# Optimization experiments

Hardware: AMD Instinct MI355X
Metric: run time of the kernel (lower is better)

## Reference

```python
import jax, jax.numpy as jnp
import numpy as np

N_NODES = 20000
N_EDGES = 320000
N_GRAPHS = 512
N_FEAT = 29
DIMS = [N_FEAT, 1024, 512, 256, 512, 1024]
EPS = 1e-5


def setup_inputs() -> dict:
    key = jax.random.key(0)
    ks = jax.random.split(key, 32)
    inp = {}
    inp["x"] = jax.random.normal(ks[0], (N_NODES, N_FEAT), dtype=jnp.float32)
    inp["edge_index"] = jax.random.randint(ks[1], (2, N_EDGES), 0, N_NODES, dtype=jnp.int64)
    inp["batch"] = jnp.sort(jax.random.randint(ks[2], (N_NODES,), 0, N_GRAPHS, dtype=jnp.int64))
    # 5 GCNConv layers: weight [in, out] + bias, plus BN gamma/beta
    for i in range(5):
        din, dout = DIMS[i], DIMS[i + 1]
        inp[f"W{i+1}"] = jax.random.normal(ks[3 + i], (din, dout), dtype=jnp.float32) * (1.0 / np.sqrt(din))
        inp[f"b{i+1}"] = jnp.zeros((dout,), dtype=jnp.float32)
        inp[f"g{i+1}"] = jnp.ones((dout,), dtype=jnp.float32)
        inp[f"be{i+1}"] = jnp.zeros((dout,), dtype=jnp.float32)
    # attention gate Linear(1024, 1)
    inp["Wg"] = jax.random.normal(ks[10], (1024, 1), dtype=jnp.float32) * 0.03
    inp["bg"] = jnp.zeros((1,), dtype=jnp.float32)
    # MLP head
    inp["Wf2"] = jax.random.normal(ks[11], (1024, 128), dtype=jnp.float32) * 0.03
    inp["bf2"] = jnp.zeros((128,), dtype=jnp.float32)
    inp["Wf3"] = jax.random.normal(ks[12], (128, 16), dtype=jnp.float32) * 0.25
    inp["bf3"] = jnp.zeros((16,), dtype=jnp.float32)
    inp["Wf4"] = jax.random.normal(ks[13], (16, 1), dtype=jnp.float32) * 0.25
    inp["bf4"] = jnp.zeros((1,), dtype=jnp.float32)
    return inp


def _gcn_conv(x, row, col, W, b):
    # PyG GCNConv: linear transform, then D^{-1/2}(A+I)D^{-1/2} aggregation, then bias.
    n = x.shape[0]
    xw = x @ W  # [N, dout]
    deg = jax.ops.segment_sum(jnp.ones_like(col, dtype=xw.dtype), col, num_segments=n)
    dinv = jnp.where(deg > 0, jax.lax.rsqrt(deg), 0.0)
    norm = dinv[row] * dinv[col]  # [E+N]
    out = jax.ops.segment_sum(xw[row] * norm[:, None], col, num_segments=n)
    return out + b


def _bn_train(x, gamma, beta):
    m = jnp.mean(x, axis=0)
    v = jnp.var(x, axis=0)  # biased, matches torch training normalization
    return gamma * (x - m) * jax.lax.rsqrt(v + EPS) + beta


def _global_attention(x, batch, Wg, bg, n_graphs):
    gate = (x @ Wg + bg)[:, 0]  # [N]
    gmax = jax.ops.segment_max(gate, batch, num_segments=n_graphs)
    e = jnp.exp(gate - gmax[batch])
    s = jax.ops.segment_sum(e, batch, num_segments=n_graphs)
    alpha = e / s[batch]
    return jax.ops.segment_sum(alpha[:, None] * x, batch, num_segments=n_graphs)


def reference(x, edge_index, batch,
              W1, b1, g1, be1, W2, b2, g2, be2, W3, b3, g3, be3,
              W4, b4, g4, be4, W5, b5, g5, be5,
              Wg, bg, Wf2, bf2, Wf3, bf3, Wf4, bf4):
    n = x.shape[0]
    sl = jnp.arange(n, dtype=edge_index.dtype)
    row = jnp.concatenate([edge_index[0], sl])  # with self-loops
    col = jnp.concatenate([edge_index[1], sl])
    h = x
    params = [(W1, b1, g1, be1), (W2, b2, g2, be2), (W3, b3, g3, be3),
              (W4, b4, g4, be4), (W5, b5, g5, be5)]
    for (W, b, g, be) in params:
        h = jax.nn.relu(_gcn_conv(h, row, col, W, b))
        h = _bn_train(h, g, be)
    p = _global_attention(h, batch, Wg, bg, N_GRAPHS)  # [G, 1024]
    p = jax.nn.relu(p @ Wf2 + bf2)
    p = jax.nn.relu(p @ Wf3 + bf3)
    return p @ Wf4 + bf4  # [G, 1]
```

## Files before the change

kernel.cpp:

```cpp
#include <hip/hip_runtime.h>

#define EPS_BN 1e-5f

constexpr int NN   = 20000;
constexpr int NE   = 320000;
constexpr int NTOT = NE + NN;
constexpr int NG   = 512;
constexpr int MPAD = 20480;
constexpr int NBLK = 79;

typedef _Float16 half8  __attribute__((ext_vector_type(8)));
typedef _Float16 half2v __attribute__((ext_vector_type(2)));
typedef float floatx4   __attribute__((ext_vector_type(4)));

__global__ void k_deg(const int* __restrict__ col, int* __restrict__ deg,
                      const int* __restrict__ batch, int* __restrict__ gcnt) {
  int e = blockIdx.x * blockDim.x + threadIdx.x;
  if (e >= NTOT) return;
  int c = (e < NE) ? col[e] : (e - NE);
  atomicAdd(&deg[c], 1);
  if (e < NN) atomicAdd(&gcnt[batch[e]], 1);
}

__global__ __launch_bounds__(256) void k_pre1(const int* __restrict__ deg,
                                              float* __restrict__ dinvv,
                                              int* __restrict__ psum) {
  __shared__ int ws[4];
  int t = threadIdx.x, lane = t & 63, wv = t >> 6;
  int idx = blockIdx.x * 256 + t;
  int d = (idx < NN) ? deg[idx] : 0;
  if (idx < NN) dinvv[idx] = rsqrtf((float)d);
  int s = d;
  for (int o = 1; o < 64; o <<= 1) { int u = __shfl_up(s, o, 64); if (lane >= o) s += u; }
  if (lane == 63) ws[wv] = s;
  __syncthreads();
  if (t == 0) psum[blockIdx.x] = ws[0] + ws[1] + ws[2] + ws[3];
}

__global__ __launch_bounds__(256) void k_pre2(const int* __restrict__ psum,
                                              int* __restrict__ pbase,
                                              const int* __restrict__ gcnt,
                                              int* __restrict__ goff) {
  __shared__ int ws[8];
  int t = threadIdx.x, lane = t & 63, wv = t >> 6;
  int v = (t < NBLK) ? psum[t] : 0;
  int inc = v;
  for (int o = 1; o < 64; o <<= 1) { int u = __shfl_up(inc, o, 64); if (lane >= o) inc += u; }
  if (lane == 63) ws[wv] = inc;
  __syncthreads();
  int base = 0;
  for (int w = 0; w < wv; ++w) base += ws[w];
  int excl = base + inc - v;
  if (t < NBLK) pbase[t] = excl;
  if (t == NBLK - 1) pbase[NBLK] = excl + v;
  __syncthreads();
  int a0 = gcnt[2 * t], a1 = gcnt[2 * t + 1];
  int p = a0 + a1;
  int incp = p;
  for (int o = 1; o < 64; o <<= 1) { int u = __shfl_up(incp, o, 64); if (lane >= o) incp += u; }
  if (lane == 63) ws[4 + wv] = incp;
  __syncthreads();
  int gb = 0;
  for (int w = 0; w < wv; ++w) gb += ws[4 + w];
  int exclp = gb + incp - p;
  goff[2 * t]     = exclp;
  goff[2 * t + 1] = exclp + a0;
  if (t == 255) goff[NG] = exclp + p;
}

__global__ __launch_bounds__(256) void k_pre3(const int* __restrict__ deg,
                                              const int* __restrict__ pbase,
                                              int* __restrict__ indptr,
                                              int* __restrict__ cursor) {
  __shared__ int ws[4];
  int t = threadIdx.x, lane = t & 63, wv = t >> 6;
  int idx = blockIdx.x * 256 + t;
  int d = (idx < NN) ? deg[idx] : 0;
  int inc = d;
  for (int o = 1; o < 64; o <<= 1) { int u = __shfl_up(inc, o, 64); if (lane >= o) inc += u; }
  if (lane == 63) ws[wv] = inc;
  __syncthreads();
  int base = pbase[blockIdx.x];
  for (int w = 0; w < wv; ++w) base += ws[w];
  int excl = base + inc - d;
  if (idx < NN) { indptr[idx] = excl; cursor[idx] = excl; }
  if (idx == NN - 1) indptr[NN] = excl + d;
}

__global__ void k_fill(const int* __restrict__ row, const int* __restrict__ col,
                       const float* __restrict__ dinv, int* __restrict__ cursor,
                       int2* __restrict__ csw, float* __restrict__ rsum) {
  int e = blockIdx.x * blockDim.x + threadIdx.x;
  if (e >= NTOT) return;
  int r, c;
  if (e < NE) { r = row[e]; c = col[e]; } else { r = c = e - NE; }
  float wv = dinv[r] * dinv[c];
  int pos = atomicAdd(&cursor[c], 1);
  int2 m; m.x = r; m.y = __builtin_bit_cast(int, wv);
  csw[pos] = m;
  atomicAdd(&rsum[c], wv);
}

__device__ __forceinline__ size_t fragoff(int n, int k, int kb) {
  return ((size_t)(n >> 4) * kb + (k >> 5)) * 512 + ((k >> 3) & 3) * 128 + (n & 15) * 8;
}

__global__ void k_wconv3(const float* __restrict__ W0, const float* __restrict__ W3,
                         const float* __restrict__ W4,
                         _Float16* __restrict__ T0, _Float16* __restrict__ T3,
                         _Float16* __restrict__ T4) {
  int c = blockIdx.x * blockDim.x + threadIdx.x;
  _Float16 ov[8];
  if (c < 4096) {
    int n = c >> 2, k = (c & 3) * 8;
    #pragma unroll
    for (int i = 0; i < 8; ++i)
      ov[i] = (_Float16)((k + i < 29) ? W0[(size_t)(k + i) * 1024 + n] : 0.f);
    *(uint4*)&T0[fragoff(n, k, 1)] = *(const uint4*)ov;
  } else if (c < 4096 + 16384) {
    int c2 = c - 4096;
    int n = c2 >> 5, k = (c2 & 31) * 8;
    #pragma unroll
    for (int i = 0; i < 8; ++i)
      ov[i] = (_Float16)W3[(size_t)(k + i) * 512 + n];
    *(uint4*)&T3[fragoff(n, k, 8)] = *(const uint4*)ov;
  } else if (c < 4096 + 16384 + 65536) {
    int c3 = c - 20480;
    int n = c3 >> 6, k = (c3 & 63) * 8;
    #pragma unroll
    for (int i = 0; i < 8; ++i)
      ov[i] = (_Float16)W4[(size_t)(k + i) * 1024 + n];
    *(uint4*)&T4[fragoff(n, k, 16)] = *(const uint4*)ov;
  }
}

__global__ __launch_bounds__(256) void k_wfold(const float* __restrict__ W, int K, int N,
                                               const float* __restrict__ sums,
                                               const float* __restrict__ gamma,
                                               const float* __restrict__ beta,
                                               _Float16* __restrict__ T,
                                               float* __restrict__ c) {
  __shared__ float red[256];
  int n = blockIdx.x, tid = threadIdx.x;
  int kb = K >> 5;
  const float inv_n = 1.f / NN;
  float csum = 0.f;
  for (int kc = tid; kc < (K >> 3); kc += 256) {
    int k = kc * 8;
    _Float16 ov[8];
    #pragma unroll
    for (int i = 0; i < 8; ++i) {
      int ki = k + i;
      float mean = sums[ki] * inv_n;
      float var  = sums[K + ki] * inv_n - mean * mean;
      float sc   = gamma[ki] * rsqrtf(var + EPS_BN);
      float sh   = beta[ki] - mean * sc;
      float wv   = W[(size_t)ki * N + n];
      ov[i] = (_Float16)(sc * wv);
      csum += sh * wv;
    }
    *(uint4*)&T[fragoff(n, k, kb)] = *(const uint4*)ov;
  }
  red[tid] = csum;
  __syncthreads();
  for (int o = 128; o > 0; o >>= 1) {
    if (tid < o) red[tid] += red[tid + o];
    __syncthreads();
  }
  if (tid == 0) c[n] = red[0];
}

#define AGG_CH 128
__global__ __launch_bounds__(128) void k_agg29(
    const float* __restrict__ X,
    const int* __restrict__ indptr, const int2* __restrict__ csw,
    _Float16* __restrict__ Y) {
  __shared__ int   s_src[AGG_CH];
  __shared__ float s_w[AGG_CH];
  __shared__ float red[128];
  int node = blockIdx.x;
  int tid  = threadIdx.x;
  int sub  = tid / 29;
  int feat = tid - sub * 29;
  bool act = tid < 116;
  int beg = indptr[node], end = indptr[node + 1];
  float acc = 0.f;
  for (int e0 = beg; e0 < end; e0 += AGG_CH) {
    int c = min(AGG_CH, end - e0);
    if (tid < c) {
      int2 m = csw[e0 + tid];
      s_src[tid] = m.x;
      s_w[tid]   = __builtin_bit_cast(float, m.y);
    }
    __syncthreads();
    if (act) {
      for (int j = 0; j < c; j += 4) {
        int jj = j + sub;
        if (jj < c) acc += s_w[jj] * X[(size_t)s_src[jj] * 29 + feat];
      }
    }
    __syncthreads();
  }
  red[tid] = acc;
  __syncthreads();
  if (tid < 32) {
    float v = 0.f;
    if (tid < 29) v = red[tid] + red[29 + tid] + red[58 + tid] + red[87 + tid];
    size_t fb = (size_t)(node >> 4) * 512 + (size_t)(tid >> 3) * 128 + (node & 15) * 8 + (tid & 7);
    Y[fb] = (_Float16)v;
  }
}

template<int MODE>
__global__ __launch_bounds__(256) void k_aggv(
    const _Float16* __restrict__ X,
    _Float16* __restrict__ Yf, _Float16* __restrict__ Yrow,
    const int* __restrict__ indptr, const int2* __restrict__ csw,
    const float* __restrict__ rowsum,
    const float* __restrict__ p0, const float* __restrict__ p1,
    const float* __restrict__ p2)
{
  constexpr int F = 512;
  int wave = threadIdx.x >> 6;
  int lane = threadIdx.x & 63;
  int node = blockIdx.x * 4 + wave;
  int beg = indptr[node], end = indptr[node + 1];
  float acc[8];
  #pragma unroll
  for (int i = 0; i < 8; ++i) acc[i] = 0.f;
  const unsigned* Xl = (const unsigned*)X + lane * 4;

  auto body = [&](int e) {
    int2 m = csw[e];
    float we = __builtin_bit_cast(float, m.y);
    uint4 d = *(const uint4*)(Xl + (size_t)m.x * (F / 2));
    unsigned uu[4] = {d.x, d.y, d.z, d.w};
    #pragma unroll
    for (int i = 0; i < 4; ++i) {
      half2v h = __builtin_bit_cast(half2v, uu[i]);
      acc[2 * i]     = fmaf(we, (float)h[0], acc[2 * i]);
      acc[2 * i + 1] = fmaf(we, (float)h[1], acc[2 * i + 1]);
    }
  };
  int e = beg;
  for (; e + 8 <= end; e += 8) {
    body(e); body(e + 1); body(e + 2); body(e + 3);
    body(e + 4); body(e + 5); body(e + 6); body(e + 7);
  }
  for (; e < end; ++e) body(e);

  float s_n = rowsum[node];
  _Float16 outv[8];
  #pragma unroll
  for (int i = 0; i < 8; ++i) {
    int f = lane * 8 + i;
    float v;
    if constexpr (MODE == 0) {
      v = fmaxf(acc[i] + s_n * p0[f] + p1[f], 0.f);
    } else {
      const float inv_n = 1.f / NN;
      float mean = p0[f] * inv_n;
      float var  = p0[F + f] * inv_n - mean * mean;
      float sc   = p1[f] * rsqrtf(var + EPS_BN);
      float sh   = p2[f] - mean * sc;
      v = sc * acc[i] + s_n * sh;
    }
    outv[i] = (_Float16)v;
  }
  if (Yf) {
    size_t fb = (size_t)(node >> 4) * (16 * 512) + lane * 128 + (node & 15) * 8;
    *(uint4*)(Yf + fb) = *(const uint4*)outv;
  }
  if (Yrow) {
    *(uint4*)(Yrow + (size_t)node * F + lane * 8) = *(const uint4*)outv;
  }
}

template<int MODE>
__global__ __launch_bounds__(256) void k_aggp(
    const _Float16* __restrict__ X,
    _Float16* __restrict__ Yf, _Float16* __restrict__ Yrow,
    const int* __restrict__ indptr, const int2* __restrict__ csw,
    const float* __restrict__ rowsum,
    const float* __restrict__ p0, const float* __restrict__ p1,
    const float* __restrict__ p2)
{
  constexpr int F = 256;
  int wave = threadIdx.x >> 6;
  int lane = threadIdx.x & 63;
  int half = lane >> 5;
  int l32  = lane & 31;
  int node = blockIdx.x * 8 + wave * 2 + half;
  int beg = indptr[node], end = indptr[node + 1];
  int len = end - beg;
  int len0 = __shfl(len, 0, 64);
  int len1 = __shfl(len, 32, 64);
  int maxlen = max(len0, len1);

  float acc[8];
  #pragma unroll
  for (int i = 0; i < 8; ++i) acc[i] = 0.f;
  const unsigned* Xl = (const unsigned*)X + l32 * 4;

  auto body = [&](int t) {
    int e = beg + min(t, len - 1);
    int2 m = csw[e];
    float we = (t < len) ? __builtin_bit_cast(float, m.y) : 0.f;
    uint4 d = *(const uint4*)(Xl + (size_t)m.x * (F / 2));
    unsigned uu[4] = {d.x, d.y, d.z, d.w};
    #pragma unroll
    for (int i = 0; i < 4; ++i) {
      half2v h = __builtin_bit_cast(half2v, uu[i]);
      acc[2 * i]     = fmaf(we, (float)h[0], acc[2 * i]);
      acc[2 * i + 1] = fmaf(we, (float)h[1], acc[2 * i + 1]);
    }
  };
  int t = 0;
  for (; t + 4 <= maxlen; t += 4) { body(t); body(t + 1); body(t + 2); body(t + 3); }
  for (; t < maxlen; ++t) body(t);

  float s_n = rowsum[node];
  _Float16 outv[8];
  #pragma unroll
  for (int i = 0; i < 8; ++i) {
    int f = l32 * 8 + i;
    float v;
    if constexpr (MODE == 0) {
      v = fmaxf(acc[i] + s_n * p0[f] + p1[f], 0.f);
    } else {
      const float inv_n = 1.f / NN;
      float mean = p0[f] * inv_n;
      float var  = p0[F + f] * inv_n - mean * mean;
      float sc   = p1[f] * rsqrtf(var + EPS_BN);
      float sh   = p2[f] - mean * sc;
      v = sc * acc[i] + s_n * sh;
    }
    outv[i] = (_Float16)v;
  }
  if (Yf) {
    size_t fb = (size_t)(node >> 4) * (8 * 512) + l32 * 128 + (node & 15) * 8;
    *(uint4*)(Yf + fb) = *(const uint4*)outv;
  }
  if (Yrow) {
    *(uint4*)(Yrow + (size_t)node * F + l32 * 8) = *(const uint4*)outv;
  }
}

template<int K, int FRAGOUT>
__global__ __launch_bounds__(256) void k_gemmf(
    const _Float16* __restrict__ Af, const _Float16* __restrict__ Bf,
    const float* __restrict__ bias,
    _Float16* __restrict__ Ch,
    _Float16* __restrict__ Cf,
    float* __restrict__ stats,
    int N, int do_relu, int nbx)
{
  __shared__ __align__(16) _Float16 cs[128 * 136];
  __shared__ float sred[256];

  const int tid  = threadIdx.x;
  const int wave = tid >> 6;
  const int lane = tid & 63;

  int lin = blockIdx.x;
  int xcd = lin & 7, seq = lin >> 3;
  int bx = seq % nbx, grp = seq / nbx;
  int by = xcd + 8 * grp;
  const int row0 = by * 128;
  const int col0 = bx * 128;

  const int q  = lane >> 4;
  const int mm = lane & 15;
  const int wm = wave >> 1;
  const int wn = wave & 1;

  sred[tid] = 0.f;

  constexpr int KB = K / 32;
  const _Float16* pa[4];
  const _Float16* pb[4];
  #pragma unroll
  for (int i = 0; i < 4; ++i)
    pa[i] = Af + (size_t)((row0 >> 4) + wm * 4 + i) * (KB * 512) + lane * 8;
  #pragma unroll
  for (int j = 0; j < 4; ++j)
    pb[j] = Bf + (size_t)((col0 >> 4) + wn * 4 + j) * (KB * 512) + lane * 8;

  floatx4 acc[4][4];
  #pragma unroll
  for (int i = 0; i < 4; ++i)
    #pragma unroll
    for (int j = 0; j < 4; ++j) acc[i][j] = floatx4{0.f, 0.f, 0.f, 0.f};

  half8 av[4], bv[4];
  #pragma unroll
  for (int i = 0; i < 4; ++i) { av[i] = *(const half8*)pa[i]; pa[i] += 512; }
  #pragma unroll
  for (int j = 0; j < 4; ++j) { bv[j] = *(const half8*)pb[j]; pb[j] += 512; }

  #pragma unroll 2
  for (int s = 0; s < KB; ++s) {
    half8 nav[4], nbv[4];
    if (s + 1 < KB) {
      #pragma unroll
      for (int i = 0; i < 4; ++i) { nav[i] = *(const half8*)pa[i]; pa[i] += 512; }
      #pragma unroll
      for (int j = 0; j < 4; ++j) { nbv[j] = *(const half8*)pb[j]; pb[j] += 512; }
    }
    #pragma unroll
    for (int j = 0; j < 4; ++j)
      #pragma unroll
      for (int i = 0; i < 4; ++i)
        acc[i][j] = __builtin_amdgcn_mfma_f32_16x16x32_f16(av[i], bv[j], acc[i][j], 0, 0, 0);
    if (s + 1 < KB) {
      #pragma unroll
      for (int i = 0; i < 4; ++i) av[i] = nav[i];
      #pragma unroll
      for (int j = 0; j < 4; ++j) bv[j] = nbv[j];
    }
  }

  __syncthreads();

  float sloc[4]  = {0.f, 0.f, 0.f, 0.f};
  float s2loc[4] = {0.f, 0.f, 0.f, 0.f};
  #pragma unroll
  for (int j = 0; j < 4; ++j) {
    int cl = wn * 64 + j * 16 + mm;
    float bvv = bias ? bias[col0 + cl] : 0.f;
    #pragma unroll
    for (int i = 0; i < 4; ++i) {
      #pragma unroll
      for (int r = 0; r < 4; ++r) {
        int rl = wm * 64 + i * 16 + q * 4 + r;
        float v = acc[i][j][r] + bvv;
        if (do_relu) v = fmaxf(v, 0.f);
        cs[rl * 136 + cl] = (_Float16)v;
        if (row0 + rl < NN) { sloc[j] += v; s2loc[j] += v * v; }
      }
    }
  }

  if (stats) {
    #pragma unroll
    for (int j = 0; j < 4; ++j) {
      float a = sloc[j], b2 = s2loc[j];
      a  += __shfl_xor(a, 16, 64);  a  += __shfl_xor(a, 32, 64);
      b2 += __shfl_xor(b2, 16, 64); b2 += __shfl_xor(b2, 32, 64);
      if (q == 0) {
        int cl = wn * 64 + j * 16 + mm;
        atomicAdd(&sred[cl], a);
        atomicAdd(&sred[128 + cl], b2);
      }
    }
  }
  __syncthreads();

  if (FRAGOUT) {
    int mlo = tid & 15, sub = (tid >> 4) & 3, kcr = (tid >> 6) & 3;
    int kbN = N >> 5;
    #pragma unroll
    for (int pass = 0; pass < 8; ++pass) {
      int m = pass * 16 + mlo;
      int kl = kcr * 32 + sub * 8;
      uint4 d = *(const uint4*)&cs[m * 136 + kl];
      size_t fa = ((size_t)((row0 >> 4) + pass) * kbN + (col0 >> 5) + kcr) * 512
                + sub * 128 + mlo * 8;
      *(uint4*)&Cf[fa] = d;
    }
  } else {
    #pragma unroll
    for (int pass = 0; pass < 8; ++pass) {
      int cidx = tid + pass * 256;
      int r = cidx >> 4, kc = cidx & 15;
      int rr = row0 + r;
      if (rr < NN) {
        uint4 d = *(const uint4*)&cs[r * 136 + kc * 8];
        *(uint4*)&Ch[(size_t)rr * N + col0 + kc * 8] = d;
      }
    }
  }

  if (stats && tid < 128) {
    atomicAdd(&stats[col0 + tid], sred[tid]);
    atomicAdd(&stats[N + col0 + tid], sred[128 + tid]);
  }
}

template<int F>
__global__ __launch_bounds__(256) void k_statsf(const _Float16* __restrict__ Xf,
                                                float* __restrict__ sums) {
  constexpr int KB = F / 32;
  constexpr int NT = NN / 16;
  int wid  = (blockIdx.x * 256 + threadIdx.x) >> 6;
  int lane = threadIdx.x & 63;
  int nw   = (gridDim.x * 256) >> 6;
  int kidx = wid % KB;
  int ng0  = wid / KB;
  int step = nw / KB;
  int sub = lane >> 4, n16 = lane & 15;

  float s[8], s2[8];
  #pragma unroll
  for (int i = 0; i < 8; ++i) { s[i] = 0.f; s2[i] = 0.f; }

  for (int ng = ng0; ng < NT; ng += step) {
    const _Float16* p = Xf + ((size_t)ng * KB + kidx) * 512 + lane * 8;
    uint4 d = *(const uint4*)p;
    unsigned uu[4] = {d.x, d.y, d.z, d.w};
    #pragma unroll
    for (int i = 0; i < 4; ++i) {
      half2v h = __builtin_bit_cast(half2v, uu[i]);
      float v0 = (float)h[0], v1 = (float)h[1];
      s[2 * i]      += v0;  s2[2 * i]     += v0 * v0;
      s[2 * i + 1]  += v1;  s2[2 * i + 1] += v1 * v1;
    }
  }
  #pragma unroll
  for (int o = 1; o < 16; o <<= 1) {
    #pragma unroll
    for (int i = 0; i < 8; ++i) {
      s[i]  += __shfl_xor(s[i],  o, 64);
      s2[i] += __shfl_xor(s2[i], o, 64);
    }
  }
  if (n16 == 0) {
    int f = kidx * 32 + sub * 8;
    #pragma unroll
    for (int i = 0; i < 8; ++i) {
      atomicAdd(&sums[f + i], s[i]);
      atomicAdd(&sums[F + f + i], s2[i]);
    }
  }
}

__global__ __launch_bounds__(256) void k_stats16(const _Float16* __restrict__ X, int F,
                                                 float* __restrict__ sums) {
  int tid = threadIdx.x;
  int npf = F >> 8;
  float s[2] = {0.f, 0.f}, s2[2] = {0.f, 0.f};
  for (int r = blockIdx.x; r < NN; r += gridDim.x) {
    #pragma unroll
    for (int i = 0; i < 2; ++i) {
      if (i < npf) {
        float v = (float)X[(size_t)r * F + tid + i * 256];
        s[i] += v; s2[i] += v * v;
      }
    }
  }
  #pragma unroll
  for (int i = 0; i < 2; ++i) {
    if (i < npf) {
      atomicAdd(&sums[tid + i * 256], s[i]);
      atomicAdd(&sums[F + tid + i * 256], s2[i]);
    }
  }
}

__global__ __launch_bounds__(256) void k_gfold(const float* __restrict__ sums,
                                               const float* __restrict__ g5,
                                               const float* __restrict__ be5,
                                               const float* __restrict__ Wg,
                                               const float* __restrict__ bg,
                                               float* __restrict__ wgf,
                                               float* __restrict__ cg) {
  __shared__ float red[256];
  int tid = threadIdx.x;
  const float inv_n = 1.f / NN;
  float t = 0.f;
  #pragma unroll
  for (int i = 0; i < 4; ++i) {
    int f = i * 256 + tid;
    float mean = sums[f] * inv_n;
    float var  = sums[1024 + f] * inv_n - mean * mean;
    float sc   = g5[f] * rsqrtf(var + EPS_BN);
    float sh   = be5[f] - mean * sc;
    float wv   = Wg[f];
    wgf[f] = sc * wv;
    t += sh * wv;
  }
  red[tid] = t;
  __syncthreads();
  for (int o = 128; o > 0; o >>= 1) {
    if (tid < o) red[tid] += red[tid + o];
    __syncthreads();
  }
  if (tid == 0) cg[0] = red[0] + bg[0];
}

__global__ __launch_bounds__(256) void k_gate3(const _Float16* __restrict__ X,
                                               const float* __restrict__ wgf,
                                               const float* __restrict__ cg,
                                               float* __restrict__ gate) {
  int wave = threadIdx.x >> 6, lane = threadIdx.x & 63;
  int node = blockIdx.x * 4 + wave;
  const _Float16* xp = X + (size_t)node * 1024 + lane * 16;
  uint4 d0 = *(const uint4*)xp;
  uint4 d1 = *(const uint4*)(xp + 8);
  const float4* wp = (const float4*)(wgf + lane * 16);
  float4 w0 = wp[0], w1 = wp[1], w2 = wp[2], w3 = wp[3];
  float wv[16] = {w0.x, w0.y, w0.z, w0.w, w1.x, w1.y, w1.z, w1.w,
                  w2.x, w2.y, w2.z, w2.w, w3.x, w3.y, w3.z, w3.w};
  unsigned uu[8] = {d0.x, d0.y, d0.z, d0.w, d1.x, d1.y, d1.z, d1.w};
  float s = 0.f;
  #pragma unroll
  for (int i = 0; i < 8; ++i) {
    half2v h = __builtin_bit_cast(half2v, uu[i]);
    s = fmaf((float)h[0], wv[2 * i],     s);
    s = fmaf((float)h[1], wv[2 * i + 1], s);
  }
  #pragma unroll
  for (int o = 1; o < 64; o <<= 1) s += __shfl_xor(s, o, 64);
  if (lane == 0) gate[node] = s + cg[0];
}

__global__ __launch_bounds__(64) void k_galpha(const int* __restrict__ goff,
                                               float* __restrict__ gate) {
  int g = blockIdx.x, lane = threadIdx.x;
  int beg = goff[g], end = goff[g + 1];
  float m = -3.4e38f;
  for (int n = beg + lane; n < end; n += 64) m = fmaxf(m, gate[n]);
  #pragma unroll
  for (int o = 1; o < 64; o <<= 1) m = fmaxf(m, __shfl_xor(m, o, 64));
  float s = 0.f;
  for (int n = beg + lane; n < end; n += 64) s += expf(gate[n] - m);
  #pragma unroll
  for (int o = 1; o < 64; o <<= 1) s += __shfl_xor(s, o, 64);
  float inv = (end > beg) ? (1.f / s) : 0.f;
  for (int n = beg + lane; n < end; n += 64) gate[n] = expf(gate[n] - m) * inv;
}

__global__ __launch_bounds__(256) void k_pool(
    const _Float16* __restrict__ X, const float* __restrict__ alpha,
    const int* __restrict__ goff,
    const float* __restrict__ sums, const float* __restrict__ g5,
    const float* __restrict__ be5,
    float* __restrict__ pooled)
{
  int g = blockIdx.x >> 2, fc = blockIdx.x & 3;
  int f = fc * 256 + threadIdx.x;
  int beg = goff[g], end = goff[g + 1];
  const _Float16* Xp = X + f;
  float acc = 0.f;
  int n = beg;
  for (; n + 4 <= end; n += 4) {
    float a0 = alpha[n], a1 = alpha[n + 1], a2 = alpha[n + 2], a3 = alpha[n + 3];
    float x0 = (float)Xp[(size_t)(n)     * 1024];
    float x1 = (float)Xp[(size_t)(n + 1) * 1024];
    float x2 = (float)Xp[(size_t)(n + 2) * 1024];
    float x3 = (float)Xp[(size_t)(n + 3) * 1024];
    acc += a0 * x0 + a1 * x1 + a2 * x2 + a3 * x3;
  }
  for (; n < end; ++n) acc += alpha[n] * (float)Xp[(size_t)n * 1024];

  const float inv_n = 1.f / NN;
  float mean = sums[f] * inv_n;
  float var  = sums[1024 + f] * inv_n - mean * mean;
  float sc   = g5[f] * rsqrtf(var + EPS_BN);
  float sh   = be5[f] - mean * sc;
  pooled[(size_t)g * 1024 + f] = (end > beg) ? (acc * sc + sh) : 0.f;
}

__global__ __launch_bounds__(256) void k_wt2(const float* __restrict__ Wf2,
                                             float* __restrict__ Wf2T) {
  int idx = blockIdx.x * 256 + threadIdx.x;
  int o = idx & 127, k = idx >> 7;
  Wf2T[(size_t)o * 1024 + k] = Wf2[idx];
}

__global__ __launch_bounds__(256) void k_head(
    const float* __restrict__ pooled,
    const float* __restrict__ Wf2T, const float* __restrict__ bf2,
    const float* __restrict__ Wf3, const float* __restrict__ bf3,
    const float* __restrict__ Wf4, const float* __restrict__ bf4,
    float* __restrict__ out)
{
  __shared__ float sp[1024];
  __shared__ float red[256];
  __shared__ float sp2[128];
  __shared__ float sp3[16];
  int g = blockIdx.x, tid = threadIdx.x;
  *(float4*)&sp[tid * 4] = *(const float4*)&pooled[(size_t)g * 1024 + tid * 4];
  __syncthreads();

  {
    int o = tid & 127, hf = tid >> 7;
    const float4* wrow = (const float4*)(Wf2T + (size_t)o * 1024 + hf * 512);
    const float* spp = &sp[hf * 512];
    float s2 = 0.f;
    #pragma unroll 4
    for (int k4 = 0; k4 < 128; ++k4) {
      float4 w = wrow[k4];
      s2 += w.x * spp[k4 * 4] + w.y * spp[k4 * 4 + 1]
          + w.z * spp[k4 * 4 + 2] + w.w * spp[k4 * 4 + 3];
    }
    red[tid] = s2;
  }
  __syncthreads();
  if (tid < 128) sp2[tid] = fmaxf(red[tid] + red[tid + 128] + bf2[tid], 0.f);
  __syncthreads();
  if (tid < 16) {
    float t = bf3[tid];
    for (int k = 0; k < 128; ++k) t += sp2[k] * Wf3[k * 16 + tid];
    sp3[tid] = fmaxf(t, 0.f);
  }
  __syncthreads();
  if (tid == 0) {
    float t = bf4[0];
    for (int k = 0; k < 16; ++k) t += sp3[k] * Wf4[k];
    out[g] = t;
  }
}

extern "C" void kernel_launch(void* const* d_in, const int* in_sizes, int n_in,
                              void* d_out, int out_size, void* d_ws, size_t ws_size,
                              hipStream_t stream) {
  const float* x     = (const float*)d_in[0];
  const int*   ei    = (const int*)d_in[1];
  const int*   batch = (const int*)d_in[2];
  const float* W[5]; const float* b[5]; const float* g[5]; const float* be[5];
  for (int l = 0; l < 5; ++l) {
    W[l]  = (const float*)d_in[3 + 4 * l];
    b[l]  = (const float*)d_in[4 + 4 * l];
    g[l]  = (const float*)d_in[5 + 4 * l];
    be[l] = (const float*)d_in[6 + 4 * l];
  }
  const float* Wg  = (const float*)d_in[23];
  const float* bg  = (const float*)d_in[24];
  const float* Wf2 = (const float*)d_in[25];
  const float* bf2 = (const float*)d_in[26];
  const float* Wf3 = (const float*)d_in[27];
  const float* bf3 = (const float*)d_in[28];
  const float* Wf4 = (const float*)d_in[29];
  const float* bf4 = (const float*)d_in[30];
  float* out = (float*)d_out;

  const int* row = ei;
  const int* col = ei + NE;

  char* base = (char*)d_ws;
  size_t off = 0;
  auto alloc = [&](size_t bytes) -> char* {
    char* p = base + off;
    off = (off + bytes + 255) & ~(size_t)255;
    return p;
  };
  _Float16*  AH  = (_Float16*)alloc((size_t)MPAD * 1024 * 2);
  _Float16*  AF  = (_Float16*)alloc((size_t)MPAD * 512 * 2);
  _Float16*  ASM = (_Float16*)alloc((size_t)MPAD * 32 * 2);
  _Float16*  BF  = (_Float16*)alloc((size_t)NN * 512 * 2);
  _Float16*  BF2 = (_Float16*)alloc((size_t)NN * 512 * 2);
  _Float16*  H5  = (_Float16*)alloc((size_t)NN * 1024 * 2);
  const int wtsz[5] = {1024 * 32, 512 * 1024, 256 * 512, 512 * 256, 1024 * 512};
  _Float16* WT[5];
  for (int l = 0; l < 5; ++l) WT[l] = (_Float16*)alloc((size_t)wtsz[l] * 2);
  float* c2  = (float*)alloc(512 * 4);
  float* c3  = (float*)alloc(256 * 4);
  float* dinv    = (float*)alloc(NN * 4);
  int*   indptr  = (int*)alloc((NN + 1) * 4);
  int*   cursor  = (int*)alloc(NN * 4);
  int2*  csw     = (int2*)alloc((size_t)NTOT * 8);
  int*   psum    = (int*)alloc((NBLK + 1) * 4);
  int*   pbase   = (int*)alloc((NBLK + 1) * 4);
  int*   goff    = (int*)alloc((NG + 1) * 4);
  float* gate    = (float*)alloc(NN * 4);
  float* wgf     = (float*)alloc(1024 * 4);
  float* cg      = (float*)alloc(4);
  float* pooled  = (float*)alloc((size_t)NG * 1024 * 4);
  float* Wf2T    = (float*)alloc((size_t)128 * 1024 * 4);
  size_t znf = 6656 + NN + NG + NN;
  float* zbase = (float*)alloc(znf * 4);
  float* bns  = zbase;
  int*   deg  = (int*)(zbase + 6656);
  int*   gcnt = (int*)(zbase + 6656 + NN);
  float* rsum = zbase + 6656 + NN + NG;
  float* bns1 = bns;
  float* bns2 = bns + 2048;
  float* bns3 = bns + 3072;
  float* bns4 = bns + 3584;
  float* bns5 = bns + 4608;

  hipMemsetAsync(zbase, 0, znf * 4, stream);
  k_deg<<<(NTOT + 255) / 256, 256, 0, stream>>>(col, deg, batch, gcnt);
  k_pre1<<<NBLK, 256, 0, stream>>>(deg, dinv, psum);
  k_pre2<<<1, 256, 0, stream>>>(psum, pbase, gcnt, goff);
  k_pre3<<<NBLK, 256, 0, stream>>>(deg, pbase, indptr, cursor);
  k_fill<<<(NTOT + 255) / 256, 256, 0, stream>>>(row, col, dinv, cursor, csw, rsum);
  k_wconv3<<<336, 256, 0, stream>>>(W[0], W[3], W[4], WT[0], WT[3], WT[4]);
  k_wt2<<<512, 256, 0, stream>>>(Wf2, Wf2T);

  k_agg29<<<NN, 128, 0, stream>>>(x, indptr, csw, ASM);
  k_gemmf<32, 1><<<8 * 160, 256, 0, stream>>>(ASM, WT[0], b[0], nullptr, AH, bns1, 1024, 1, 8);

  k_wfold<<<512, 256, 0, stream>>>(W[1], 1024, 512, bns1, g[0], be[0], WT[1], c2);
  k_gemmf<1024, 0><<<4 * 160, 256, 0, stream>>>(AH, WT[1], nullptr, BF, nullptr, nullptr, 512, 0, 4);
  k_aggv<0><<<NN / 4, 256, 0, stream>>>(BF, AF, nullptr, indptr, csw, rsum, c2, b[1], nullptr);
  k_statsf<512><<<256, 256, 0, stream>>>(AF, bns2);

  k_wfold<<<256, 256, 0, stream>>>(W[2], 512, 256, bns2, g[1], be[1], WT[2], c3);
  k_gemmf<512, 0><<<2 * 160, 256, 0, stream>>>(AF, WT[2], nullptr, BF2, nullptr, nullptr, 256, 0, 2);
  k_aggp<0><<<NN / 8, 256, 0, stream>>>(BF2, nullptr, BF, indptr, csw, rsum, c3, b[2], nullptr);
  k_stats16<<<512, 256, 0, stream>>>(BF, 256, bns3);

  k_aggp<1><<<NN / 8, 256, 0, stream>>>(BF, AH, nullptr, indptr, csw, rsum, bns3, g[2], be[2]);
  k_gemmf<256, 0><<<4 * 160, 256, 0, stream>>>(AH, WT[3], b[3], BF2, nullptr, bns4, 512, 1, 4);

  k_aggv<1><<<NN / 4, 256, 0, stream>>>(BF2, AF, nullptr, indptr, csw, rsum, bns4, g[3], be[3]);
  k_gemmf<512, 0><<<8 * 160, 256, 0, stream>>>(AF, WT[4], b[4], H5, nullptr, bns5, 1024, 1, 8);

  k_gfold<<<1, 256, 0, stream>>>(bns5, g[4], be[4], Wg, bg, wgf, cg);
  k_gate3<<<NN / 4, 256, 0, stream>>>(H5, wgf, cg, gate);
  k_galpha<<<NG, 64, 0, stream>>>(goff, gate);
  k_pool<<<NG * 4, 256, 0, stream>>>(H5, gate, goff, bns5, g[4], be[4], pooled);
  k_head<<<NG, 256, 0, stream>>>(pooled, Wf2T, bf2, Wf3, bf3, Wf4, bf4, out);
}
```

Baseline: 597.5 us.

## Unify sparse aggregation kernels with feature-chunked, edge-parallel quarter-waves

Replaces the two aggregation kernels with one templated kernel. Each wave handles one node and a 128-feature chunk, and its four 16-lane groups each take a different edge, with the partial sums combined by cross-lane shuffles. Feature chunks become separate blocks, which multiplies the block count, and outputs are written with nontemporal stores. The aim is more memory-level parallelism per node and less lane idling from uneven degrees. In exchange, the edge index and weight reads are repeated for every chunk, and a shuffle reduction is added.

```diff
diff --git a/kernel.cpp b/kernel.cpp
--- a/kernel.cpp
+++ b/kernel.cpp
@@ -12,6 +12,7 @@
 typedef _Float16 half8  __attribute__((ext_vector_type(8)));
 typedef _Float16 half2v __attribute__((ext_vector_type(2)));
 typedef float floatx4   __attribute__((ext_vector_type(4)));
+typedef unsigned int uintx4 __attribute__((ext_vector_type(4)));
 
 __global__ void k_deg(const int* __restrict__ col, int* __restrict__ deg,
                       const int* __restrict__ batch, int* __restrict__ gcnt) {
@@ -211,8 +212,8 @@
   }
 }
 
-template<int MODE>
-__global__ __launch_bounds__(256) void k_aggv(
+template<int F, int MODE>
+__global__ __launch_bounds__(256) void k_aggc(
     const _Float16* __restrict__ X,
     _Float16* __restrict__ Yf, _Float16* __restrict__ Yrow,
     const int* __restrict__ indptr, const int2* __restrict__ csw,
@@ -220,20 +221,30 @@
     const float* __restrict__ p0, const float* __restrict__ p1,
     const float* __restrict__ p2)
 {
-  constexpr int F = 512;
+  constexpr int NB = NN / 4;
+  int bid  = blockIdx.x;
+  int c    = bid / NB;
+  int nb   = bid - c * NB;
   int wave = threadIdx.x >> 6;
   int lane = threadIdx.x & 63;
-  int node = blockIdx.x * 4 + wave;
-  int beg = indptr[node], end = indptr[node + 1];
+  int q    = lane >> 4;
+  int l    = lane & 15;
+  int node = nb * 4 + wave;
+  int beg  = indptr[node];
+  int len  = indptr[node + 1] - beg;
+
+  const _Float16* Xc = X + c * 128 + l * 8;
+
   float acc[8];
   #pragma unroll
   for (int i = 0; i < 8; ++i) acc[i] = 0.f;
-  const unsigned* Xl = (const unsigned*)X + lane * 4;
-
-  auto body = [&](int e) {
+
+  auto body = [&](int t) {
+    int ee = t * 4 + q;
+    int e  = beg + min(ee, len - 1);
     int2 m = csw[e];
-    float we = __builtin_bit_cast(float, m.y);
-    uint4 d = *(const uint4*)(Xl + (size_t)m.x * (F / 2));
+    float we = (ee < len) ? __builtin_bit_cast(float, m.y) : 0.f;
+    uint4 d = *(const uint4*)(Xc + (size_t)m.x * F);
     unsigned uu[4] = {d.x, d.y, d.z, d.w};
     #pragma unroll
     for (int i = 0; i < 4; ++i) {
@@ -242,18 +253,22 @@
       acc[2 * i + 1] = fmaf(we, (float)h[1], acc[2 * i + 1]);
     }
   };
-  int e = beg;
-  for (; e + 8 <= end; e += 8) {
-    body(e); body(e + 1); body(e + 2); body(e + 3);
-    body(e + 4); body(e + 5); body(e + 6); body(e + 7);
-  }
-  for (; e < end; ++e) body(e);
+  int nstep = (len + 3) >> 2;
+  int t = 0;
+  for (; t + 4 <= nstep; t += 4) { body(t); body(t + 1); body(t + 2); body(t + 3); }
+  for (; t < nstep; ++t) body(t);
+
+  #pragma unroll
+  for (int i = 0; i < 8; ++i) {
+    acc[i] += __shfl_xor(acc[i], 16, 64);
+    acc[i] += __shfl_xor(acc[i], 32, 64);
+  }
 
   float s_n = rowsum[node];
-  _Float16 outv[8];
+  half8 outv;
   #pragma unroll
   for (int i = 0; i < 8; ++i) {
-    int f = lane * 8 + i;
+    int f = c * 128 + l * 8 + i;
     float v;
     if constexpr (MODE == 0) {
       v = fmaxf(acc[i] + s_n * p0[f] + p1[f], 0.f);
@@ -267,82 +282,15 @@
     }
     outv[i] = (_Float16)v;
   }
-  if (Yf) {
-    size_t fb = (size_t)(node >> 4) * (16 * 512) + lane * 128 + (node & 15) * 8;
-    *(uint4*)(Yf + fb) = *(const uint4*)outv;
-  }
-  if (Yrow) {
-    *(uint4*)(Yrow + (size_t)node * F + lane * 8) = *(const uint4*)outv;
-  }
-}
-
-template<int MODE>
-__global__ __launch_bounds__(256) void k_aggp(
-    const _Float16* __restrict__ X,
-    _Float16* __restrict__ Yf, _Float16* __restrict__ Yrow,
-    const int* __restrict__ indptr, const int2* __restrict__ csw,
-    const float* __restrict__ rowsum,
-    const float* __restrict__ p0, const float* __restrict__ p1,
-    const float* __restrict__ p2)
-{
-  constexpr int F = 256;
-  int wave = threadIdx.x >> 6;
-  int lane = threadIdx.x & 63;
-  int half = lane >> 5;
-  int l32  = lane & 31;
-  int node = blockIdx.x * 8 + wave * 2 + half;
-  int beg = indptr[node], end = indptr[node + 1];
-  int len = end - beg;
-  int len0 = __shfl(len, 0, 64);
-  int len1 = __shfl(len, 32, 64);
-  int maxlen = max(len0, len1);
-
-  float acc[8];
-  #pragma unroll
-  for (int i = 0; i < 8; ++i) acc[i] = 0.f;
-  const unsigned* Xl = (const unsigned*)X + l32 * 4;
-
-  auto body = [&](int t) {
-    int e = beg + min(t, len - 1);
-    int2 m = csw[e];
-    float we = (t < len) ? __builtin_bit_cast(float, m.y) : 0.f;
-    uint4 d = *(const uint4*)(Xl + (size_t)m.x * (F / 2));
-    unsigned uu[4] = {d.x, d.y, d.z, d.w};
-    #pragma unroll
-    for (int i = 0; i < 4; ++i) {
-      half2v h = __builtin_bit_cast(half2v, uu[i]);
-      acc[2 * i]     = fmaf(we, (float)h[0], acc[2 * i]);
-      acc[2 * i + 1] = fmaf(we, (float)h[1], acc[2 * i + 1]);
-    }
-  };
-  int t = 0;
-  for (; t + 4 <= maxlen; t += 4) { body(t); body(t + 1); body(t + 2); body(t + 3); }
-  for (; t < maxlen; ++t) body(t);
-
-  float s_n = rowsum[node];
-  _Float16 outv[8];
-  #pragma unroll
-  for (int i = 0; i < 8; ++i) {
-    int f = l32 * 8 + i;
-    float v;
-    if constexpr (MODE == 0) {
-      v = fmaxf(acc[i] + s_n * p0[f] + p1[f], 0.f);
-    } else {
-      const float inv_n = 1.f / NN;
-      float mean = p0[f] * inv_n;
-      float var  = p0[F + f] * inv_n - mean * mean;
-      float sc   = p1[f] * rsqrtf(var + EPS_BN);
-      float sh   = p2[f] - mean * sc;
-      v = sc * acc[i] + s_n * sh;
-    }
-    outv[i] = (_Float16)v;
-  }
-  if (Yf) {
-    size_t fb = (size_t)(node >> 4) * (8 * 512) + l32 * 128 + (node & 15) * 8;
-    *(uint4*)(Yf + fb) = *(const uint4*)outv;
-  }
-  if (Yrow) {
-    *(uint4*)(Yrow + (size_t)node * F + l32 * 8) = *(const uint4*)outv;
+  if (q == 0) {
+    uintx4 uv = __builtin_bit_cast(uintx4, outv);
+    if (Yf) {
+      size_t fb = (size_t)(node >> 4) * ((F / 32) * 512) + c * 2048 + l * 128 + (node & 15) * 8;
+      __builtin_nontemporal_store(uv, (uintx4*)(Yf + fb));
+    }
+    if (Yrow) {
+      __builtin_nontemporal_store(uv, (uintx4*)(Yrow + (size_t)node * F + c * 128 + l * 8));
+    }
   }
 }
 
@@ -794,18 +742,18 @@
 
   k_wfold<<<512, 256, 0, stream>>>(W[1], 1024, 512, bns1, g[0], be[0], WT[1], c2);
   k_gemmf<1024, 0><<<4 * 160, 256, 0, stream>>>(AH, WT[1], nullptr, BF, nullptr, nullptr, 512, 0, 4);
-  k_aggv<0><<<NN / 4, 256, 0, stream>>>(BF, AF, nullptr, indptr, csw, rsum, c2, b[1], nullptr);
+  k_aggc<512, 0><<<4 * (NN / 4), 256, 0, stream>>>(BF, AF, nullptr, indptr, csw, rsum, c2, b[1], nullptr);
   k_statsf<512><<<256, 256, 0, stream>>>(AF, bns2);
 
   k_wfold<<<256, 256, 0, stream>>>(W[2], 512, 256, bns2, g[1], be[1], WT[2], c3);
   k_gemmf<512, 0><<<2 * 160, 256, 0, stream>>>(AF, WT[2], nullptr, BF2, nullptr, nullptr, 256, 0, 2);
-  k_aggp<0><<<NN / 8, 256, 0, stream>>>(BF2, nullptr, BF, indptr, csw, rsum, c3, b[2], nullptr);
+  k_aggc<256, 0><<<2 * (NN / 4), 256, 0, stream>>>(BF2, nullptr, BF, indptr, csw, rsum, c3, b[2], nullptr);
   k_stats16<<<512, 256, 0, stream>>>(BF, 256, bns3);
 
-  k_aggp<1><<<NN / 8, 256, 0, stream>>>(BF, AH, nullptr, indptr, csw, rsum, bns3, g[2], be[2]);
+  k_aggc<256, 1><<<2 * (NN / 4), 256, 0, stream>>>(BF, AH, nullptr, indptr, csw, rsum, bns3, g[2], be[2]);
   k_gemmf<256, 0><<<4 * 160, 256, 0, stream>>>(AH, WT[3], b[3], BF2, nullptr, bns4, 512, 1, 4);
 
-  k_aggv<1><<<NN / 4, 256, 0, stream>>>(BF2, AF, nullptr, indptr, csw, rsum, bns4, g[3], be[3]);
+  k_aggc<512, 1><<<4 * (NN / 4), 256, 0, stream>>>(BF2, AF, nullptr, indptr, csw, rsum, bns4, g[3], be[3]);
   k_gemmf<512, 0><<<8 * 160, 256, 0, stream>>>(AF, WT[4], b[4], H5, nullptr, bns5, 1024, 1, 8);
 
   k_gfold<<<1, 256, 0, stream>>>(bns5, g[4], be[4], Wg, bg, wgf, cg);
```

Result: slower. 609.7 us (+2.0%).

## Add direct global-to-LDS GEMM kernel for layer-2 and layer-5 GEMMs

Applied to the files above, without the earlier changes.

Introduces k_gemmf3, a 128x128-tile MFMA GEMM that stages fragment-layout A and B tiles into shared memory with global_load_lds. This bypasses the register round-trip on the load path. It is used for the 1024->512 GEMM and for the 512->1024 GEMM with bias, ReLU and BN statistics. The K loop has a single buffer with two barriers per 64-wide step, so latency hiding depends on occupancy rather than software pipelining. fragoff gains a (k&7) term, which is zero at the existing call sites.

```diff
diff --git a/kernel.cpp b/kernel.cpp
--- a/kernel.cpp
+++ b/kernel.cpp
@@ -102,7 +102,7 @@
 }
 
 __device__ __forceinline__ size_t fragoff(int n, int k, int kb) {
-  return ((size_t)(n >> 4) * kb + (k >> 5)) * 512 + ((k >> 3) & 3) * 128 + (n & 15) * 8;
+  return ((size_t)(n >> 4) * kb + (k >> 5)) * 512 + ((k >> 3) & 3) * 128 + (n & 15) * 8 + (k & 7);
 }
 
 __global__ void k_wconv3(const float* __restrict__ W0, const float* __restrict__ W3,
@@ -478,6 +478,137 @@
         uint4 d = *(const uint4*)&cs[r * 136 + kc * 8];
         *(uint4*)&Ch[(size_t)rr * N + col0 + kc * 8] = d;
       }
+    }
+  }
+
+  if (stats && tid < 128) {
+    atomicAdd(&stats[col0 + tid], sred[tid]);
+    atomicAdd(&stats[N + col0 + tid], sred[128 + tid]);
+  }
+}
+
+template<int K>
+__global__ __launch_bounds__(256) void k_gemmf3(
+    const _Float16* __restrict__ Af, const _Float16* __restrict__ Bf,
+    const float* __restrict__ bias,
+    _Float16* __restrict__ Ch,
+    float* __restrict__ stats,
+    int N, int do_relu, int nbx)
+{
+  constexpr int KB = K / 32;
+  constexpr int NS = K / 64;
+  __shared__ __align__(16) _Float16 smem[128 * 136];
+  __shared__ float sred[256];
+
+  const int tid  = threadIdx.x;
+  const int wave = tid >> 6;
+  const int lane = tid & 63;
+
+  int lin = blockIdx.x;
+  int xcd = lin & 7, seq = lin >> 3;
+  int bx = seq % nbx, grp = seq / nbx;
+  int by = xcd + 8 * grp;
+  const int row0 = by * 128;
+  const int col0 = bx * 128;
+
+  const int q  = lane >> 4;
+  const int mm = lane & 15;
+  const int wm = wave >> 1;
+  const int wn = wave & 1;
+
+  sred[tid] = 0.f;
+
+  _Float16* ldsA = smem;
+  _Float16* ldsB = smem + 8192;
+
+  floatx4 acc[4][4];
+  #pragma unroll
+  for (int i = 0; i < 4; ++i)
+    #pragma unroll
+    for (int j = 0; j < 4; ++j) acc[i][j] = floatx4{0.f, 0.f, 0.f, 0.f};
+
+  const int sh  = wave & 1;
+  const int frb = wave >> 1;
+
+  for (int s = 0; s < NS; ++s) {
+    #pragma unroll
+    for (int p = 0; p < 4; ++p) {
+      int fr = 2 * p + frb;
+      const _Float16* sa = Af + ((size_t)((row0 >> 4) + fr) * KB + 2 * s) * 512
+                         + sh * 512 + lane * 8;
+      __builtin_amdgcn_global_load_lds(
+          (const __attribute__((address_space(1))) void*)sa,
+          (__attribute__((address_space(3))) void*)&ldsA[fr * 1024 + sh * 512],
+          16, 0, 0);
+      const _Float16* sb = Bf + ((size_t)((col0 >> 4) + fr) * KB + 2 * s) * 512
+                         + sh * 512 + lane * 8;
+      __builtin_amdgcn_global_load_lds(
+          (const __attribute__((address_space(1))) void*)sb,
+          (__attribute__((address_space(3))) void*)&ldsB[fr * 1024 + sh * 512],
+          16, 0, 0);
+    }
+    __syncthreads();
+    #pragma unroll
+    for (int kk = 0; kk < 2; ++kk) {
+      half8 av[4], bv[4];
+      #pragma unroll
+      for (int i = 0; i < 4; ++i)
+        av[i] = *(const half8*)&ldsA[((wm * 4 + i) * 2 + kk) * 512 + lane * 8];
+      #pragma unroll
+      for (int j = 0; j < 4; ++j)
+        bv[j] = *(const half8*)&ldsB[((wn * 4 + j) * 2 + kk) * 512 + lane * 8];
+      #pragma unroll
+      for (int j = 0; j < 4; ++j)
+        #pragma unroll
+        for (int i = 0; i < 4; ++i)
+          acc[i][j] = __builtin_amdgcn_mfma_f32_16x16x32_f16(av[i], bv[j], acc[i][j], 0, 0, 0);
+    }
+    __syncthreads();
+  }
+
+  _Float16* cs = smem;
+  float sloc[4]  = {0.f, 0.f, 0.f, 0.f};
+  float s2loc[4] = {0.f, 0.f, 0.f, 0.f};
+  #pragma unroll
+  for (int j = 0; j < 4; ++j) {
+    int cl = wn * 64 + j * 16 + mm;
+    float bvv = bias ? bias[col0 + cl] : 0.f;
+    #pragma unroll
+    for (int i = 0; i < 4; ++i) {
+      #pragma unroll
+      for (int r = 0; r < 4; ++r) {
+        int rl = wm * 64 + i * 16 + q * 4 + r;
+        float v = acc[i][j][r] + bvv;
+        if (do_relu) v = fmaxf(v, 0.f);
+        cs[rl * 136 + cl] = (_Float16)v;
+        if (row0 + rl < NN) { sloc[j] += v; s2loc[j] += v * v; }
+      }
+    }
+  }
+
+  if (stats) {
+    #pragma unroll
+    for (int j = 0; j < 4; ++j) {
+      float a = sloc[j], b2 = s2loc[j];
+      a  += __shfl_xor(a, 16, 64);  a  += __shfl_xor(a, 32, 64);
+      b2 += __shfl_xor(b2, 16, 64); b2 += __shfl_xor(b2, 32, 64);
+      if (q == 0) {
+        int cl = wn * 64 + j * 16 + mm;
+        atomicAdd(&sred[cl], a);
+        atomicAdd(&sred[128 + cl], b2);
+      }
+    }
+  }
+  __syncthreads();
+
+  #pragma unroll
+  for (int pass = 0; pass < 8; ++pass) {
+    int cidx = tid + pass * 256;
+    int r = cidx >> 4, kc = cidx & 15;
+    int rr = row0 + r;
+    if (rr < NN) {
+      uint4 d = *(const uint4*)&cs[r * 136 + kc * 8];
+      *(uint4*)&Ch[(size_t)rr * N + col0 + kc * 8] = d;
     }
   }
 
@@ -793,7 +924,7 @@
   k_gemmf<32, 1><<<8 * 160, 256, 0, stream>>>(ASM, WT[0], b[0], nullptr, AH, bns1, 1024, 1, 8);
 
   k_wfold<<<512, 256, 0, stream>>>(W[1], 1024, 512, bns1, g[0], be[0], WT[1], c2);
-  k_gemmf<1024, 0><<<4 * 160, 256, 0, stream>>>(AH, WT[1], nullptr, BF, nullptr, nullptr, 512, 0, 4);
+  k_gemmf3<1024><<<4 * 160, 256, 0, stream>>>(AH, WT[1], nullptr, BF, nullptr, 512, 0, 4);
   k_aggv<0><<<NN / 4, 256, 0, stream>>>(BF, AF, nullptr, indptr, csw, rsum, c2, b[1], nullptr);
   k_statsf<512><<<256, 256, 0, stream>>>(AF, bns2);
 
@@ -806,7 +937,7 @@
   k_gemmf<256, 0><<<4 * 160, 256, 0, stream>>>(AH, WT[3], b[3], BF2, nullptr, bns4, 512, 1, 4);
 
   k_aggv<1><<<NN / 4, 256, 0, stream>>>(BF2, AF, nullptr, indptr, csw, rsum, bns4, g[3], be[3]);
-  k_gemmf<512, 0><<<8 * 160, 256, 0, stream>>>(AF, WT[4], b[4], H5, nullptr, bns5, 1024, 1, 8);
+  k_gemmf3<512><<<8 * 160, 256, 0, stream>>>(AF, WT[4], b[4], H5, bns5, 1024, 1, 8);
 
   k_gfold<<<1, 256, 0, stream>>>(bns5, g[4], be[4], Wg, bg, wgf, cg);
   k_gate3<<<NN / 4, 256, 0, stream>>>(H5, wgf, cg, gate);
```

New measurement: 582.4 us. 1.03x faster.
